# Kernel tuning notes

Measured on AMD Instinct MI355X. Metric: run time of the kernel, lower is better.

The kernel has to match this reference:

```python
import jax, jax.numpy as jnp
import numpy as np

B, L, D = 2048, 200, 256
N_USERS, N_ATTRS, N_RATINGS = 100000, 50000, 5


def setup_inputs() -> dict:
    key = jax.random.key(0)
    ks = jax.random.split(key, 16)
    s = 0.02
    return {
        "nodes": jax.random.randint(ks[0], (B,), 0, N_USERS),
        "history_ua": jax.random.randint(ks[1], (B, L), 0, N_ATTRS),
        "history_r": jax.random.randint(ks[2], (B, L), 0, N_RATINGS),
        "history_uat": jax.random.randint(ks[3], (B, L), 0, 512),
        "u2e_w": jax.random.normal(ks[4], (N_USERS, D), jnp.float32) * s,
        "attr_w": jax.random.normal(ks[5], (N_ATTRS, D), jnp.float32) * s,
        "r2e_w": jax.random.normal(ks[6], (N_RATINGS, D), jnp.float32) * s,
        "w_r1_w": jax.random.normal(ks[7], (D, 2 * D), jnp.float32) * s,
        "w_r1_b": jnp.zeros((D,), jnp.float32),
        "w_r2_w": jax.random.normal(ks[8], (D, D), jnp.float32) * s,
        "w_r2_b": jnp.zeros((D,), jnp.float32),
        "att1_w": jax.random.normal(ks[9], (D, 2 * D), jnp.float32) * s,
        "att1_b": jnp.zeros((D,), jnp.float32),
        "att2_w": jax.random.normal(ks[10], (D, D), jnp.float32) * s,
        "att2_b": jnp.zeros((D,), jnp.float32),
        "att3_w": jax.random.normal(ks[11], (1, D), jnp.float32) * s,
        "att3_b": jnp.zeros((1,), jnp.float32),
    }


def reference(nodes, history_ua, history_r, history_uat,
              u2e_w, attr_w, r2e_w,
              w_r1_w, w_r1_b, w_r2_w, w_r2_b,
              att1_w, att1_b, att2_w, att2_b, att3_w, att3_b):
    # gathers: e_ua [B,L,D], e_r [B,L,D], ua_rep [B,D]
    e_ua = attr_w[history_ua]
    e_r = r2e_w[history_r]
    ua_rep = u2e_w[nodes]
    # o_history = relu(w_r2(relu(w_r1(cat(e_ua, e_r)))))  [B,L,D]
    x = jnp.concatenate([e_ua, e_r], axis=-1)            # [B,L,2D]
    x = jax.nn.relu(jnp.einsum('bld,kd->blk', x, w_r1_w) + w_r1_b)
    o = jax.nn.relu(jnp.einsum('bld,kd->blk', x, w_r2_w) + w_r2_b)
    # attention: MLP on cat(o_history, ua_rep) -> softmax over history dim
    a = jnp.concatenate([o, jnp.broadcast_to(ua_rep[:, None, :], o.shape)], axis=-1)  # [B,L,2D]
    h = jax.nn.relu(jnp.einsum('bld,kd->blk', a, att1_w) + att1_b)
    h = jax.nn.relu(jnp.einsum('bld,kd->blk', h, att2_w) + att2_b)
    score = jnp.einsum('bld,kd->blk', h, att3_w) + att3_b  # [B,L,1]
    att = jax.nn.softmax(score, axis=1)
    # weighted reduce: o^T @ att per node -> [B,D]
    return jnp.sum(o * att, axis=1)
```

## Files before the change

kernel.cpp:

```cpp
#include <hip/hip_runtime.h>
#include <hip/hip_bf16.h>

typedef __bf16 bf16;
typedef __bf16 bf16x8 __attribute__((ext_vector_type(8)));
typedef float f32x4 __attribute__((ext_vector_type(4)));

#define L_SZ 200
#define D_SZ 256
#define NROWS (2048 * 200)
#define MB 128
#define MB2 64
#define AST 264
#define N_ATTR 50000
#define NPB ((N_ATTR + MB - 1) / MB)

#define WS_W2F 0u
#define WS_A1L 131072u
#define WS_A1H 262144u
#define WS_A2F 393216u
#define WS_W1A 524288u
#define WS_W1F 655360u
#define WS_R   917504u
#define WS_H1P 925696u
#define WS_SCR 3022848u
#define WS_O   4661248u
#define WS_P   214376448u
#define WS_NEED_OLD 214376448u
#define WS_NEED_NEW 239976448u

__device__ __forceinline__ void swz_one(const float* __restrict__ W, bf16* __restrict__ dst,
                                        int KT, int ldw, int koff, int g) {
    int lane = g & 63;
    int kt = (g >> 6) % KT;
    int nt = g / (64 * KT);
    int n = nt * 16 + (lane & 15);
    int k = kt * 32 + (lane >> 4) * 8;
    const float* src = W + (long)n * ldw + koff + k;
    f32x4 a = *(const f32x4*)src;
    f32x4 b = *(const f32x4*)(src + 4);
    bf16x8 v;
    v[0] = (bf16)a[0]; v[1] = (bf16)a[1]; v[2] = (bf16)a[2]; v[3] = (bf16)a[3];
    v[4] = (bf16)b[0]; v[5] = (bf16)b[1]; v[6] = (bf16)b[2]; v[7] = (bf16)b[3];
    *(bf16x8*)(dst + (long)g * 8) = v;
}

__global__ void swizzle_kernel(const float* __restrict__ W, bf16* __restrict__ dst,
                               int KT, int ldw, int koff, int total) {
    int g = blockIdx.x * blockDim.x + threadIdx.x;
    if (g >= total) return;
    swz_one(W, dst, KT, ldw, koff, g);
}

__global__ void swizzle_all(const float* __restrict__ w2, const float* __restrict__ a1w,
                            const float* __restrict__ a2w, const float* __restrict__ w1,
                            bf16* __restrict__ wf_w2, bf16* __restrict__ wf_a1l,
                            bf16* __restrict__ wf_a2f, bf16* __restrict__ wf_a1h,
                            bf16* __restrict__ wf_w1a,
                            const float* __restrict__ r2e, const float* __restrict__ b1w,
                            float* __restrict__ Rg) {
    __shared__ float e[5 * D_SZ];
    const int blk = blockIdx.x, t = threadIdx.x;
    if (blk == 160) {
        for (int i = t; i < 5 * D_SZ; i += 256) e[i] = r2e[i];
        __syncthreads();
        const float* wr = w1 + (long)t * 512 + 256;
        float bb = b1w[t];
        for (int r = 0; r < 5; ++r) {
            float a = bb;
            const float* er = e + r * D_SZ;
#pragma unroll
            for (int k = 0; k < D_SZ; k += 4) {
                f32x4 wv = *(const f32x4*)(wr + k);
                a += er[k] * wv[0] + er[k + 1] * wv[1] + er[k + 2] * wv[2] + er[k + 3] * wv[3];
            }
            Rg[r * D_SZ + t] = a;
        }
        return;
    }
    int job = blk >> 5, lb = blk & 31;
    int g = lb * 256 + t;
    const float* W; bf16* dst; int ldw, koff;
    switch (job) {
        case 0:  W = w2;  dst = wf_w2;  ldw = 256; koff = 0;   break;
        case 1:  W = a1w; dst = wf_a1l; ldw = 512; koff = 0;   break;
        case 2:  W = a2w; dst = wf_a2f; ldw = 256; koff = 0;   break;
        case 3:  W = a1w; dst = wf_a1h; ldw = 512; koff = 256; break;
        default: W = w1;  dst = wf_w1a; ldw = 512; koff = 0;   break;
    }
    swz_one(W, dst, 8, ldw, koff, g);
}

__device__ __forceinline__ void stage_rows(const int* __restrict__ idxl,
                                           const float* __restrict__ table,
                                           bf16* __restrict__ buf, int t) {
#pragma unroll
    for (int it = 0; it < 16; ++it) {
        int g = it * 256 + t;
        int r = g >> 5;
        int c = g & 31;
        long row = idxl[r];
        const float* f = table + row * D_SZ + c * 8;
        f32x4 a = *(const f32x4*)f;
        f32x4 b = *(const f32x4*)(f + 4);
        bf16x8 v;
        v[0] = (bf16)a[0]; v[1] = (bf16)a[1]; v[2] = (bf16)a[2]; v[3] = (bf16)a[3];
        v[4] = (bf16)b[0]; v[5] = (bf16)b[1]; v[6] = (bf16)b[2]; v[7] = (bf16)b[3];
        *(bf16x8*)(buf + r * AST + c * 8) = v;
    }
}

template <int MT, int KTOT>
__device__ __forceinline__ void gemm_t(const bf16* __restrict__ abase,
                                       const bf16* __restrict__ wfrag, int koff_t,
                                       int wave, int lane, int l16, int quad,
                                       f32x4 (&acc)[MT][4]) {
    const bf16* wbase = wfrag + ((long)(wave * 4) * KTOT + koff_t) * 512 + lane * 8;
    bf16x8 bc[4], bn[4];
#pragma unroll
    for (int nt = 0; nt < 4; ++nt)
        bc[nt] = *(const bf16x8*)(wbase + (long)nt * KTOT * 512);
#pragma unroll
    for (int kt = 0; kt < 8; ++kt) {
        if (kt < 7) {
#pragma unroll
            for (int nt = 0; nt < 4; ++nt)
                bn[nt] = *(const bf16x8*)(wbase + ((long)nt * KTOT + kt + 1) * 512);
        }
        bf16x8 a[MT];
#pragma unroll
        for (int mt = 0; mt < MT; ++mt)
            a[mt] = *(const bf16x8*)(abase + (mt * 16 + l16) * AST + kt * 32 + quad * 8);
#pragma unroll
        for (int nt = 0; nt < 4; ++nt)
#pragma unroll
            for (int mt = 0; mt < MT; ++mt)
                acc[mt][nt] = __builtin_amdgcn_mfma_f32_16x16x32_bf16(a[mt], bc[nt], acc[mt][nt], 0, 0, 0);
#pragma unroll
        for (int nt = 0; nt < 4; ++nt) bc[nt] = bn[nt];
    }
}

template <int MT>
__device__ __forceinline__ void zero_t(f32x4 (&acc)[MT][4]) {
    f32x4 z = {0.f, 0.f, 0.f, 0.f};
#pragma unroll
    for (int mt = 0; mt < MT; ++mt)
#pragma unroll
        for (int nt = 0; nt < 4; ++nt) acc[mt][nt] = z;
}

template <int MT>
__device__ __forceinline__ void store_act_t(bf16* __restrict__ buf, f32x4 (&acc)[MT][4],
                                            const float* bias, int wave, int l16, int quad) {
#pragma unroll
    for (int mt = 0; mt < MT; ++mt)
#pragma unroll
        for (int nt = 0; nt < 4; ++nt) {
            int col = (wave * 4 + nt) * 16 + l16;
#pragma unroll
            for (int r = 0; r < 4; ++r) {
                int row = mt * 16 + quad * 4 + r;
                float v = acc[mt][nt][r] + bias[nt];
                v = v > 0.f ? v : 0.f;
                buf[row * AST + col] = (bf16)v;
            }
        }
}

__device__ __forceinline__ void store_lin8(bf16* __restrict__ buf, f32x4 (&acc)[8][4],
                                           int wave, int l16, int quad) {
#pragma unroll
    for (int mt = 0; mt < 8; ++mt)
#pragma unroll
        for (int nt = 0; nt < 4; ++nt) {
            int col = (wave * 4 + nt) * 16 + l16;
#pragma unroll
            for (int r = 0; r < 4; ++r) {
                int row = mt * 16 + quad * 4 + r;
                buf[row * AST + col] = (bf16)acc[mt][nt][r];
            }
        }
}

__launch_bounds__(256, 2)
__global__ void kpre_k0(const float* __restrict__ attr, const bf16* __restrict__ wf_w1a,
                        bf16* __restrict__ Pt,
                        const int* __restrict__ nodes, const float* __restrict__ u2e,
                        const bf16* __restrict__ wf_a1h, const float* __restrict__ a1b,
                        float* __restrict__ h1p) {
    __shared__ __align__(16) bf16 abuf[MB * AST];
    __shared__ int idxl[MB];
    const int blk = blockIdx.x, t = threadIdx.x;
    const int wave = t >> 6, lane = t & 63, l16 = t & 15, quad = (t & 63) >> 4;
    const bool isP = blk < NPB;
    if (t < MB) {
        if (isP) { int r = blk * MB + t; idxl[t] = r < N_ATTR ? r : (N_ATTR - 1); }
        else idxl[t] = nodes[(blk - NPB) * MB + t];
    }
    __syncthreads();
    stage_rows(idxl, isP ? attr : u2e, abuf, t);
    __syncthreads();
    f32x4 acc[8][4];
    zero_t<8>(acc);
    gemm_t<8, 8>(abuf, isP ? wf_w1a : wf_a1h, 0, wave, lane, l16, quad, acc);
    if (isP) {
        __syncthreads();
        store_lin8(abuf, acc, wave, l16, quad);
        __syncthreads();
#pragma unroll
        for (int it = 0; it < 16; ++it) {
            int g = it * 256 + t;
            int r = g >> 5, c = g & 31;
            long row = (long)blk * MB + r;
            if (row < N_ATTR)
                *(bf16x8*)(Pt + row * D_SZ + c * 8) = *(const bf16x8*)(abuf + r * AST + c * 8);
        }
    } else {
        const int blk0 = blk - NPB;
#pragma unroll
        for (int nt = 0; nt < 4; ++nt) {
            int col = (wave * 4 + nt) * 16 + l16;
            float ab = a1b[col];
#pragma unroll
            for (int mt = 0; mt < 8; ++mt)
#pragma unroll
                for (int r = 0; r < 4; ++r) {
                    int row = mt * 16 + quad * 4 + r;
                    h1p[(long)(blk0 * MB + row) * D_SZ + col] = acc[mt][nt][r] + ab;
                }
        }
    }
}

__launch_bounds__(256, 2)
__global__ void k0_h1pre(const int* __restrict__ nodes, const float* __restrict__ u2e,
                         const bf16* __restrict__ wf_a1h, const float* __restrict__ a1b,
                         float* __restrict__ h1p) {
    __shared__ __align__(16) bf16 abuf[MB * AST];
    __shared__ int idxl[MB];
    const int blk = blockIdx.x, t = threadIdx.x;
    const int wave = t >> 6, lane = t & 63, l16 = t & 15, quad = (t & 63) >> 4;
    if (t < MB) idxl[t] = nodes[blk * MB + t];
    __syncthreads();
    stage_rows(idxl, u2e, abuf, t);
    __syncthreads();
    f32x4 acc[8][4];
    zero_t<8>(acc);
    gemm_t<8, 8>(abuf, wf_a1h, 0, wave, lane, l16, quad, acc);
#pragma unroll
    for (int nt = 0; nt < 4; ++nt) {
        int col = (wave * 4 + nt) * 16 + l16;
        float ab = a1b[col];
#pragma unroll
        for (int mt = 0; mt < 8; ++mt)
#pragma unroll
            for (int r = 0; r < 4; ++r) {
                int row = mt * 16 + quad * 4 + r;
                h1p[(long)(blk * MB + row) * D_SZ + col] = acc[mt][nt][r] + ab;
            }
    }
}

__launch_bounds__(256, 4)
__global__ void k1f_fused(const int* __restrict__ hua, const int* __restrict__ hr,
                          const bf16* __restrict__ Pt, const float* __restrict__ Rg,
                          const bf16* __restrict__ wf_w2, const bf16* __restrict__ wf_a1l,
                          const bf16* __restrict__ wf_a2f, const float* __restrict__ h1p,
                          const float* __restrict__ b2w, const float* __restrict__ a2b,
                          const float* __restrict__ a3w,
                          bf16* __restrict__ o_out, float* __restrict__ scores) {
    __shared__ __align__(16) bf16 abuf[MB2 * AST];
    __shared__ int idx_ua[MB2], idx_r[MB2];
    __shared__ float Rl[5 * D_SZ];
    __shared__ float spart[4][MB2];
    const int blk = blockIdx.x, t = threadIdx.x;
    const int wave = t >> 6, lane = t & 63, l16 = t & 15, quad = (t & 63) >> 4;
    const long r0 = (long)blk * MB2;
    const int b0 = (int)(r0 / L_SZ);
    const int b1i = min(b0 + 1, 2047);
    const long bsplit = (long)(b0 + 1) * L_SZ;
    if (t < MB2) { idx_ua[t] = hua[r0 + t]; idx_r[t] = hr[r0 + t]; }
    for (int i = t; i < 5 * D_SZ; i += 256) Rl[i] = Rg[i];
    __syncthreads();
#pragma unroll
    for (int it = 0; it < 4; ++it) {
        int g = it * 256 + t;
        int r = g >> 4, c = g & 15;
        long row = idx_ua[r];
        const bf16* pp = Pt + row * D_SZ + c * 16;
        bf16x8 v0 = *(const bf16x8*)pp;
        bf16x8 v1 = *(const bf16x8*)(pp + 8);
        const float* Rr = Rl + idx_r[r] * D_SZ + c * 16;
        f32x4 ra = *(const f32x4*)(Rr);
        f32x4 rb = *(const f32x4*)(Rr + 4);
        f32x4 rc = *(const f32x4*)(Rr + 8);
        f32x4 rd = *(const f32x4*)(Rr + 12);
        bf16x8 o0, o1;
#pragma unroll
        for (int j = 0; j < 4; ++j) {
            float a = (float)v0[j] + ra[j];
            float b = (float)v0[j + 4] + rb[j];
            float cc = (float)v1[j] + rc[j];
            float d = (float)v1[j + 4] + rd[j];
            o0[j]     = (bf16)(a > 0.f ? a : 0.f);
            o0[j + 4] = (bf16)(b > 0.f ? b : 0.f);
            o1[j]     = (bf16)(cc > 0.f ? cc : 0.f);
            o1[j + 4] = (bf16)(d > 0.f ? d : 0.f);
        }
        *(bf16x8*)(abuf + r * AST + c * 16) = o0;
        *(bf16x8*)(abuf + r * AST + c * 16 + 8) = o1;
    }
    __syncthreads();

    f32x4 acc[4][4];
    zero_t<4>(acc);
    gemm_t<4, 8>(abuf, wf_w2, 0, wave, lane, l16, quad, acc);
    __syncthreads();
    float bias2[4];
#pragma unroll
    for (int nt = 0; nt < 4; ++nt) bias2[nt] = b2w[(wave * 4 + nt) * 16 + l16];
    store_act_t<4>(abuf, acc, bias2, wave, l16, quad);
    __syncthreads();
#pragma unroll
    for (int it = 0; it < 8; ++it) {
        int g = it * 256 + t;
        int r = g >> 5, c = g & 31;
        *(bf16x8*)(o_out + (r0 + r) * D_SZ + c * 8) = *(const bf16x8*)(abuf + r * AST + c * 8);
    }
    zero_t<4>(acc);
    gemm_t<4, 8>(abuf, wf_a1l, 0, wave, lane, l16, quad, acc);
    __syncthreads();
    float h0v[4], h1v[4];
#pragma unroll
    for (int nt = 0; nt < 4; ++nt) {
        int col = (wave * 4 + nt) * 16 + l16;
        h0v[nt] = h1p[(long)b0 * D_SZ + col];
        h1v[nt] = h1p[(long)b1i * D_SZ + col];
    }
#pragma unroll
    for (int nt = 0; nt < 4; ++nt) {
        int col = (wave * 4 + nt) * 16 + l16;
#pragma unroll
        for (int mt = 0; mt < 4; ++mt)
#pragma unroll
            for (int r = 0; r < 4; ++r) {
                int row = mt * 16 + quad * 4 + r;
                float bias = ((r0 + row) >= bsplit) ? h1v[nt] : h0v[nt];
                float v = acc[mt][nt][r] + bias;
                v = v > 0.f ? v : 0.f;
                abuf[row * AST + col] = (bf16)v;
            }
    }
    __syncthreads();
    zero_t<4>(acc);
    gemm_t<4, 8>(abuf, wf_a2f, 0, wave, lane, l16, quad, acc);

    float bias4[4], a3[4];
#pragma unroll
    for (int nt = 0; nt < 4; ++nt) {
        int col = (wave * 4 + nt) * 16 + l16;
        bias4[nt] = a2b[col];
        a3[nt] = a3w[col];
    }
    float p[4][4];
#pragma unroll
    for (int mt = 0; mt < 4; ++mt)
#pragma unroll
        for (int r = 0; r < 4; ++r) {
            float s = 0.f;
#pragma unroll
            for (int nt = 0; nt < 4; ++nt) {
                float h = acc[mt][nt][r] + bias4[nt];
                h = h > 0.f ? h : 0.f;
                s += h * a3[nt];
            }
            p[mt][r] = s;
        }
#pragma unroll
    for (int off = 1; off < 16; off <<= 1)
#pragma unroll
        for (int mt = 0; mt < 4; ++mt)
#pragma unroll
            for (int r = 0; r < 4; ++r) p[mt][r] += __shfl_xor(p[mt][r], off, 16);
    if (l16 == 0) {
#pragma unroll
        for (int mt = 0; mt < 4; ++mt)
#pragma unroll
            for (int r = 0; r < 4; ++r)
                spart[wave][mt * 16 + quad * 4 + r] = p[mt][r];
    }
    __syncthreads();
    if (t < MB2)
        scores[r0 + t] = spart[0][t] + spart[1][t] + spart[2][t] + spart[3][t];
}

__launch_bounds__(256, 2)
__global__ void k1_gemm12(const int* __restrict__ hua, const int* __restrict__ hr,
                          const float* __restrict__ attr, const float* __restrict__ r2e,
                          const bf16* __restrict__ wf_w1, const bf16* __restrict__ wf_w2,
                          const float* __restrict__ b1w, const float* __restrict__ b2w,
                          bf16* __restrict__ o_out) {
    __shared__ __align__(16) bf16 abuf[MB * AST];
    __shared__ int idx_ua[MB], idx_r[MB];
    const int blk = blockIdx.x, t = threadIdx.x;
    const int wave = t >> 6, lane = t & 63, l16 = t & 15, quad = (t & 63) >> 4;
    const long r0 = (long)blk * MB;
    if (t < MB) { idx_ua[t] = hua[r0 + t]; idx_r[t] = hr[r0 + t]; }
    __syncthreads();

    float bias1[4], bias2[4];
#pragma unroll
    for (int nt = 0; nt < 4; ++nt) {
        int col = (wave * 4 + nt) * 16 + l16;
        bias1[nt] = b1w[col];
        bias2[nt] = b2w[col];
    }

    f32x4 acc[8][4];
    zero_t<8>(acc);
    stage_rows(idx_ua, attr, abuf, t);
    __syncthreads();
    gemm_t<8, 16>(abuf, wf_w1, 0, wave, lane, l16, quad, acc);
    __syncthreads();
    stage_rows(idx_r, r2e, abuf, t);
    __syncthreads();
    gemm_t<8, 16>(abuf, wf_w1, 8, wave, lane, l16, quad, acc);
    __syncthreads();
    store_act_t<8>(abuf, acc, bias1, wave, l16, quad);
    __syncthreads();
    zero_t<8>(acc);
    gemm_t<8, 8>(abuf, wf_w2, 0, wave, lane, l16, quad, acc);
    __syncthreads();
    store_act_t<8>(abuf, acc, bias2, wave, l16, quad);
    __syncthreads();
#pragma unroll
    for (int it = 0; it < 16; ++it) {
        int g = it * 256 + t;
        int r = g >> 5, c = g & 31;
        *(bf16x8*)(o_out + (r0 + r) * D_SZ + c * 8) = *(const bf16x8*)(abuf + r * AST + c * 8);
    }
}

__launch_bounds__(256, 2)
__global__ void k2_gemm34(const bf16* __restrict__ o_in,
                          const bf16* __restrict__ wf_a1l, const bf16* __restrict__ wf_a2f,
                          const float* __restrict__ h1p, const float* __restrict__ a2b,
                          const float* __restrict__ a3w, float* __restrict__ scores) {
    __shared__ __align__(16) bf16 abuf[MB * AST];
    __shared__ float hp[2][D_SZ];
    __shared__ float spart[4][MB];
    const int blk = blockIdx.x, t = threadIdx.x;
    const int wave = t >> 6, lane = t & 63, l16 = t & 15, quad = (t & 63) >> 4;
    const long r0 = (long)blk * MB;
    const int b0 = (int)(r0 / L_SZ);
    const int b1 = min(b0 + 1, 2047);
    const long bsplit = (long)(b0 + 1) * L_SZ;
    hp[0][t] = h1p[(long)b0 * D_SZ + t];
    hp[1][t] = h1p[(long)b1 * D_SZ + t];
#pragma unroll
    for (int it = 0; it < 16; ++it) {
        int g = it * 256 + t;
        int r = g >> 5, c = g & 31;
        *(bf16x8*)(abuf + r * AST + c * 8) = *(const bf16x8*)(o_in + (r0 + r) * D_SZ + c * 8);
    }
    __syncthreads();

    f32x4 acc[8][4];
    zero_t<8>(acc);
    gemm_t<8, 8>(abuf, wf_a1l, 0, wave, lane, l16, quad, acc);
    __syncthreads();
#pragma unroll
    for (int nt = 0; nt < 4; ++nt) {
        int col = (wave * 4 + nt) * 16 + l16;
#pragma unroll
        for (int mt = 0; mt < 8; ++mt)
#pragma unroll
            for (int r = 0; r < 4; ++r) {
                int row = mt * 16 + quad * 4 + r;
                float bias = ((r0 + row) >= bsplit) ? hp[1][col] : hp[0][col];
                float v = acc[mt][nt][r] + bias;
                v = v > 0.f ? v : 0.f;
                abuf[row * AST + col] = (bf16)v;
            }
    }
    __syncthreads();
    zero_t<8>(acc);
    gemm_t<8, 8>(abuf, wf_a2f, 0, wave, lane, l16, quad, acc);

    float bias4[4], a3[4];
#pragma unroll
    for (int nt = 0; nt < 4; ++nt) {
        int col = (wave * 4 + nt) * 16 + l16;
        bias4[nt] = a2b[col];
        a3[nt] = a3w[col];
    }
    float p[8][4];
#pragma unroll
    for (int mt = 0; mt < 8; ++mt)
#pragma unroll
        for (int r = 0; r < 4; ++r) {
            float s = 0.f;
#pragma unroll
            for (int nt = 0; nt < 4; ++nt) {
                float h = acc[mt][nt][r] + bias4[nt];
                h = h > 0.f ? h : 0.f;
                s += h * a3[nt];
            }
            p[mt][r] = s;
        }
#pragma unroll
    for (int off = 1; off < 16; off <<= 1)
#pragma unroll
        for (int mt = 0; mt < 8; ++mt)
#pragma unroll
            for (int r = 0; r < 4; ++r) p[mt][r] += __shfl_xor(p[mt][r], off, 16);
    if (l16 == 0) {
#pragma unroll
        for (int mt = 0; mt < 8; ++mt)
#pragma unroll
            for (int r = 0; r < 4; ++r)
                spart[wave][mt * 16 + quad * 4 + r] = p[mt][r];
    }
    __syncthreads();
    if (t < MB)
        scores[r0 + t] = spart[0][t] + spart[1][t] + spart[2][t] + spart[3][t];
}

__global__ void k5_reduce(const float* __restrict__ scores, const bf16* __restrict__ o_in,
                          float* __restrict__ out) {
    __shared__ float red[256];
    __shared__ float watt[256];
    __shared__ float racc[8][264];
    const int b = blockIdx.x, t = threadIdx.x;
    float s = (t < L_SZ) ? scores[(long)b * L_SZ + t] : -INFINITY;
    red[t] = s;
    __syncthreads();
    for (int off = 128; off > 0; off >>= 1) {
        if (t < off) red[t] = fmaxf(red[t], red[t + off]);
        __syncthreads();
    }
    float mx = red[0];
    __syncthreads();
    float w = (t < L_SZ) ? __expf(s - mx) : 0.f;
    watt[t] = w;
    red[t] = w;
    __syncthreads();
    for (int off = 128; off > 0; off >>= 1) {
        if (t < off) red[t] += red[t + off];
        __syncthreads();
    }
    float inv = 1.f / red[0];
    const int c8 = t & 31, rg = t >> 5;
    f32x4 a0 = {0.f, 0.f, 0.f, 0.f}, a1 = {0.f, 0.f, 0.f, 0.f};
    const bf16* ob = o_in + (long)b * L_SZ * D_SZ + c8 * 8;
#pragma unroll 5
    for (int l = rg; l < L_SZ; l += 8) {
        float wv = watt[l];
        bf16x8 v = *(const bf16x8*)(ob + (long)l * D_SZ);
        a0[0] += wv * (float)v[0]; a0[1] += wv * (float)v[1];
        a0[2] += wv * (float)v[2]; a0[3] += wv * (float)v[3];
        a1[0] += wv * (float)v[4]; a1[1] += wv * (float)v[5];
        a1[2] += wv * (float)v[6]; a1[3] += wv * (float)v[7];
    }
    *(f32x4*)(&racc[rg][c8 * 8]) = a0;
    *(f32x4*)(&racc[rg][c8 * 8 + 4]) = a1;
    __syncthreads();
    float r2 = 0.f;
#pragma unroll
    for (int g = 0; g < 8; ++g) r2 += racc[g][t];
    out[(long)b * D_SZ + t] = r2 * inv;
}

__device__ __forceinline__ void gather_half_f(const int* __restrict__ idxp,
                                              const float* __restrict__ table,
                                              bf16* __restrict__ buf, int l0, int t) {
#pragma unroll
    for (int it = 0; it < 6; ++it) {
        int g = it * 256 + t;
        int r = g >> 5, c = g & 31;
        int l = l0 + r;
        int li = l < L_SZ ? l : (L_SZ - 1);
        long row = idxp[li];
        const float* f = table + row * D_SZ + c * 8;
        f32x4 a = *(const f32x4*)f;
        f32x4 b2 = *(const f32x4*)(f + 4);
        bf16x8 v;
        v[0] = (bf16)a[0]; v[1] = (bf16)a[1]; v[2] = (bf16)a[2]; v[3] = (bf16)a[3];
        v[4] = (bf16)b2[0]; v[5] = (bf16)b2[1]; v[6] = (bf16)b2[2]; v[7] = (bf16)b2[3];
        *(bf16x8*)(buf + r * AST + c * 8) = v;
    }
}

__launch_bounds__(256, 3)
__global__ void ua_fused(const int* __restrict__ nodes, const int* __restrict__ hua,
                         const int* __restrict__ hr, const float* __restrict__ u2e,
                         const float* __restrict__ attr, const float* __restrict__ r2e,
                         const bf16* __restrict__ wf1, const bf16* __restrict__ wf2,
                         const bf16* __restrict__ wfa1, const bf16* __restrict__ wfa2,
                         const float* __restrict__ b1w, const float* __restrict__ b2w,
                         const float* __restrict__ att1w, const float* __restrict__ a1b,
                         const float* __restrict__ a2b, const float* __restrict__ att3w,
                         const float* __restrict__ a3bp, float* __restrict__ out) {
    __shared__ __align__(16) bf16 abuf[48 * AST];
    __shared__ __align__(16) bf16 obuf[48 * AST];
    __shared__ float h1pre[D_SZ];
    __shared__ float scratch[288];
    const int b = blockIdx.x, t = threadIdx.x;
    const int wave = t >> 6, lane = t & 63, l16 = t & 15, quad = (t & 63) >> 4;
    {
        int node = nodes[b];
        scratch[t] = u2e[(long)node * D_SZ + t];
        __syncthreads();
        float a = a1b[t];
        const float* wr = att1w + (long)t * 512 + 256;
#pragma unroll
        for (int k = 0; k < 256; k += 4) {
            f32x4 wv = *(const f32x4*)(wr + k);
            a += scratch[k] * wv[0] + scratch[k + 1] * wv[1] +
                 scratch[k + 2] * wv[2] + scratch[k + 3] * wv[3];
        }
        h1pre[t] = a;
        __syncthreads();
    }
    float bias1[4], bias2[4], bias3[4], bias4[4], a3[4];
#pragma unroll
    for (int nt = 0; nt < 4; ++nt) {
        int col = (wave * 4 + nt) * 16 + l16;
        bias1[nt] = b1w[col]; bias2[nt] = b2w[col]; bias3[nt] = h1pre[col];
        bias4[nt] = a2b[col]; a3[nt] = att3w[col];
    }
    const float a3bias = a3bp[0];
    const int* huab = hua + (long)b * L_SZ;
    const int* hrb = hr + (long)b * L_SZ;
    float accv = 0.f, srun = 0.f, mrun = -INFINITY;
    float* score_part = scratch;
    float* score_row = scratch + 192;
    float* wrow = scratch + 240;
    auto st3 = [&](bf16* buf, f32x4 (&acc)[3][4], const float* bias) {
#pragma unroll
        for (int mt = 0; mt < 3; ++mt)
#pragma unroll
            for (int nt = 0; nt < 4; ++nt) {
                int col = (wave * 4 + nt) * 16 + l16;
#pragma unroll
                for (int r = 0; r < 4; ++r) {
                    float v = acc[mt][nt][r] + bias[nt];
                    v = v > 0.f ? v : 0.f;
                    buf[(mt * 16 + quad * 4 + r) * AST + col] = (bf16)v;
                }
            }
    };
    for (int tile = 0; tile < 5; ++tile) {
        const int l0 = tile * 48;
        f32x4 acc[3][4];
        zero_t<3>(acc);
        gather_half_f(huab, attr, abuf, l0, t);
        __syncthreads();
        gemm_t<3, 16>(abuf, wf1, 0, wave, lane, l16, quad, acc);
        __syncthreads();
        gather_half_f(hrb, r2e, abuf, l0, t);
        __syncthreads();
        gemm_t<3, 16>(abuf, wf1, 8, wave, lane, l16, quad, acc);
        __syncthreads();
        st3(abuf, acc, bias1);
        __syncthreads();
        zero_t<3>(acc);
        gemm_t<3, 8>(abuf, wf2, 0, wave, lane, l16, quad, acc);
        st3(obuf, acc, bias2);
        __syncthreads();
        zero_t<3>(acc);
        gemm_t<3, 8>(obuf, wfa1, 0, wave, lane, l16, quad, acc);
        st3(abuf, acc, bias3);
        __syncthreads();
        zero_t<3>(acc);
        gemm_t<3, 8>(abuf, wfa2, 0, wave, lane, l16, quad, acc);
        float p[3][4];
#pragma unroll
        for (int mt = 0; mt < 3; ++mt)
#pragma unroll
            for (int r = 0; r < 4; ++r) {
                float s = 0.f;
#pragma unroll
                for (int nt = 0; nt < 4; ++nt) {
                    float h = acc[mt][nt][r] + bias4[nt];
                    h = h > 0.f ? h : 0.f;
                    s += h * a3[nt];
                }
                p[mt][r] = s;
            }
#pragma unroll
        for (int off = 1; off < 16; off <<= 1)
#pragma unroll
            for (int mt = 0; mt < 3; ++mt)
#pragma unroll
                for (int r = 0; r < 4; ++r) p[mt][r] += __shfl_xor(p[mt][r], off, 16);
        if (l16 == 0) {
#pragma unroll
            for (int mt = 0; mt < 3; ++mt)
#pragma unroll
                for (int r = 0; r < 4; ++r)
                    score_part[wave * 48 + mt * 16 + quad * 4 + r] = p[mt][r];
        }
        __syncthreads();
        if (t < 48) {
            float s = score_part[t] + score_part[48 + t] + score_part[96 + t] +
                      score_part[144 + t] + a3bias;
            score_row[t] = (l0 + t < L_SZ) ? s : -INFINITY;
        }
        __syncthreads();
        float tm = -INFINITY;
        for (int r = 0; r < 48; ++r) tm = fmaxf(tm, score_row[r]);
        float nm = fmaxf(mrun, tm);
        float factor = __expf(mrun - nm);
        if (t < 48) wrow[t] = __expf(score_row[t] - nm);
        __syncthreads();
        float wsum = 0.f, av = 0.f;
#pragma unroll 8
        for (int r = 0; r < 48; ++r) {
            float w = wrow[r];
            wsum += w;
            av += w * (float)obuf[r * AST + t];
        }
        accv = accv * factor + av;
        srun = srun * factor + wsum;
        mrun = nm;
        __syncthreads();
    }
    out[(long)b * D_SZ + t] = accv / srun;
}

extern "C" void kernel_launch(void* const* d_in, const int* in_sizes, int n_in,
                              void* d_out, int out_size, void* d_ws, size_t ws_size,
                              hipStream_t stream) {
    const int* nodes = (const int*)d_in[0];
    const int* hua = (const int*)d_in[1];
    const int* hr = (const int*)d_in[2];
    const float* u2e = (const float*)d_in[4];
    const float* attr = (const float*)d_in[5];
    const float* r2e = (const float*)d_in[6];
    const float* w1 = (const float*)d_in[7];
    const float* b1 = (const float*)d_in[8];
    const float* w2 = (const float*)d_in[9];
    const float* b2 = (const float*)d_in[10];
    const float* a1w = (const float*)d_in[11];
    const float* a1b = (const float*)d_in[12];
    const float* a2w = (const float*)d_in[13];
    const float* a2b = (const float*)d_in[14];
    const float* a3w = (const float*)d_in[15];
    const float* a3b = (const float*)d_in[16];
    char* ws = (char*)d_ws;
    bf16* wf_w2 = (bf16*)(ws + WS_W2F);
    bf16* wf_a1l = (bf16*)(ws + WS_A1L);
    bf16* wf_a1h = (bf16*)(ws + WS_A1H);
    bf16* wf_a2f = (bf16*)(ws + WS_A2F);
    bf16* wf_w1a = (bf16*)(ws + WS_W1A);
    bf16* wf_w1 = (bf16*)(ws + WS_W1F);

    if (ws_size >= (size_t)WS_NEED_NEW) {
        float* Rg = (float*)(ws + WS_R);
        float* h1p = (float*)(ws + WS_H1P);
        float* scores = (float*)(ws + WS_SCR);
        bf16* obuf = (bf16*)(ws + WS_O);
        bf16* Pt = (bf16*)(ws + WS_P);
        swizzle_all<<<161, 256, 0, stream>>>(w2, a1w, a2w, w1,
                                             wf_w2, wf_a1l, wf_a2f, wf_a1h, wf_w1a,
                                             r2e, b1, Rg);
        kpre_k0<<<NPB + 2048 / MB, 256, 0, stream>>>(attr, wf_w1a, Pt,
                                                     nodes, u2e, wf_a1h, a1b, h1p);
        k1f_fused<<<NROWS / MB2, 256, 0, stream>>>(hua, hr, Pt, Rg, wf_w2, wf_a1l,
                                                   wf_a2f, h1p, b2, a2b, a3w,
                                                   obuf, scores);
        k5_reduce<<<2048, 256, 0, stream>>>(scores, obuf, (float*)d_out);
    } else if (ws_size >= (size_t)WS_NEED_OLD) {
        float* h1p = (float*)(ws + WS_H1P);
        float* scores = (float*)(ws + WS_SCR);
        bf16* obuf = (bf16*)(ws + WS_O);
        swizzle_kernel<<<32, 256, 0, stream>>>(w2, wf_w2, 8, 256, 0, 8192);
        swizzle_kernel<<<32, 256, 0, stream>>>(a1w, wf_a1l, 8, 512, 0, 8192);
        swizzle_kernel<<<32, 256, 0, stream>>>(a2w, wf_a2f, 8, 256, 0, 8192);
        swizzle_kernel<<<64, 256, 0, stream>>>(w1, wf_w1, 16, 512, 0, 16384);
        swizzle_kernel<<<32, 256, 0, stream>>>(a1w, wf_a1h, 8, 512, 256, 8192);
        k0_h1pre<<<2048 / MB, 256, 0, stream>>>(nodes, u2e, wf_a1h, a1b, h1p);
        k1_gemm12<<<NROWS / MB, 256, 0, stream>>>(hua, hr, attr, r2e, wf_w1, wf_w2,
                                                  b1, b2, obuf);
        k2_gemm34<<<NROWS / MB, 256, 0, stream>>>(obuf, wf_a1l, wf_a2f, h1p, a2b,
                                                  a3w, scores);
        k5_reduce<<<2048, 256, 0, stream>>>(scores, obuf, (float*)d_out);
    } else {
        swizzle_kernel<<<32, 256, 0, stream>>>(w2, wf_w2, 8, 256, 0, 8192);
        swizzle_kernel<<<32, 256, 0, stream>>>(a1w, wf_a1l, 8, 512, 0, 8192);
        swizzle_kernel<<<32, 256, 0, stream>>>(a2w, wf_a2f, 8, 256, 0, 8192);
        swizzle_kernel<<<64, 256, 0, stream>>>(w1, wf_w1, 16, 512, 0, 16384);
        ua_fused<<<2048, 256, 0, stream>>>(nodes, hua, hr, u2e, attr, r2e,
                                           wf_w1, wf_w2, wf_a1l, wf_a2f,
                                           b1, b2, a1w, a1b, a2b, a3w, a3b,
                                           (float*)d_out);
    }
}
```

Measured before the change: 526.5 us.

## Fuse softmax-weighted reduction into fused kernel via per-block partial stats

The fused MLP kernel no longer writes the bf16 o_history buffer and per-row scores to global memory. Each 64-row block now keeps o in packed registers, computes a local max and exp-sum for each of the two batch segments it spans, and writes weighted partial sums plus stats. A small combine kernel merges these flash-style into the output. The precompute kernel also moves to 64-row tiles with direct fp32→bf16 staging and higher occupancy, and the fused kernel reads R from global memory instead of LDS. The cost is extra registers for the packed o copy and the added shuffle reductions.

New measurement: 576.6 us. 1.1x slower.

```diff
diff --git a/kernel.cpp b/kernel.cpp
--- a/kernel.cpp
+++ b/kernel.cpp
@@ -13,6 +13,8 @@
 #define AST 264
 #define N_ATTR 50000
 #define NPB ((N_ATTR + MB - 1) / MB)
+#define NPB64 ((N_ATTR + MB2 - 1) / MB2)
+#define NK0 (2048 / MB2)
 
 #define WS_W2F 0u
 #define WS_A1L 131072u
@@ -24,9 +26,21 @@
 #define WS_H1P 925696u
 #define WS_SCR 3022848u
 #define WS_O   4661248u
+#define WS_PART 4661248u
+#define WS_STAT 17768448u
 #define WS_P   214376448u
 #define WS_NEED_OLD 214376448u
 #define WS_NEED_NEW 239976448u
+
+__device__ __forceinline__ unsigned pack2(float a, float b) {
+    unsigned short ua = __builtin_bit_cast(unsigned short, (bf16)a);
+    unsigned short ub = __builtin_bit_cast(unsigned short, (bf16)b);
+    return (unsigned)ua | ((unsigned)ub << 16);
+}
+__device__ __forceinline__ float unpk(unsigned v, int hi) {
+    unsigned short u = hi ? (unsigned short)(v >> 16) : (unsigned short)(v & 0xffff);
+    return (float)__builtin_bit_cast(bf16, u);
+}
 
 __device__ __forceinline__ void swz_one(const float* __restrict__ W, bf16* __restrict__ dst,
                                         int KT, int ldw, int koff, int g) {
@@ -167,10 +181,32 @@
         }
 }
 
-__device__ __forceinline__ void store_lin8(bf16* __restrict__ buf, f32x4 (&acc)[8][4],
-                                           int wave, int l16, int quad) {
-#pragma unroll
-    for (int mt = 0; mt < 8; ++mt)
+__device__ __forceinline__ void store_act_pack4(bf16* __restrict__ buf, f32x4 (&acc)[4][4],
+                                                const float* bias, unsigned (&obak)[4][4][2],
+                                                int wave, int l16, int quad) {
+#pragma unroll
+    for (int mt = 0; mt < 4; ++mt)
+#pragma unroll
+        for (int nt = 0; nt < 4; ++nt) {
+            int col = (wave * 4 + nt) * 16 + l16;
+            float v[4];
+#pragma unroll
+            for (int r = 0; r < 4; ++r) {
+                float x = acc[mt][nt][r] + bias[nt];
+                v[r] = x > 0.f ? x : 0.f;
+                int row = mt * 16 + quad * 4 + r;
+                buf[row * AST + col] = (bf16)v[r];
+            }
+            obak[mt][nt][0] = pack2(v[0], v[1]);
+            obak[mt][nt][1] = pack2(v[2], v[3]);
+        }
+}
+
+template <int MT>
+__device__ __forceinline__ void store_lin_t(bf16* __restrict__ buf, f32x4 (&acc)[MT][4],
+                                            int wave, int l16, int quad) {
+#pragma unroll
+    for (int mt = 0; mt < MT; ++mt)
 #pragma unroll
         for (int nt = 0; nt < 4; ++nt) {
             int col = (wave * 4 + nt) * 16 + l16;
@@ -182,54 +218,274 @@
         }
 }
 
-__launch_bounds__(256, 2)
+__launch_bounds__(256, 4)
 __global__ void kpre_k0(const float* __restrict__ attr, const bf16* __restrict__ wf_w1a,
                         bf16* __restrict__ Pt,
                         const int* __restrict__ nodes, const float* __restrict__ u2e,
                         const bf16* __restrict__ wf_a1h, const float* __restrict__ a1b,
                         float* __restrict__ h1p) {
-    __shared__ __align__(16) bf16 abuf[MB * AST];
-    __shared__ int idxl[MB];
+    __shared__ __align__(16) bf16 abuf[MB2 * AST];
     const int blk = blockIdx.x, t = threadIdx.x;
     const int wave = t >> 6, lane = t & 63, l16 = t & 15, quad = (t & 63) >> 4;
-    const bool isP = blk < NPB;
-    if (t < MB) {
-        if (isP) { int r = blk * MB + t; idxl[t] = r < N_ATTR ? r : (N_ATTR - 1); }
-        else idxl[t] = nodes[(blk - NPB) * MB + t];
-    }
-    __syncthreads();
-    stage_rows(idxl, isP ? attr : u2e, abuf, t);
-    __syncthreads();
-    f32x4 acc[8][4];
-    zero_t<8>(acc);
-    gemm_t<8, 8>(abuf, isP ? wf_w1a : wf_a1h, 0, wave, lane, l16, quad, acc);
+    const bool isP = blk < NPB64;
+    const int blk0 = blk - NPB64;
+    const float* table = isP ? attr : u2e;
+#pragma unroll
+    for (int it = 0; it < 8; ++it) {
+        int g = it * 256 + t;
+        int r = g >> 5, c = g & 31;
+        long row;
+        if (isP) { row = (long)blk * MB2 + r; if (row >= N_ATTR) row = N_ATTR - 1; }
+        else row = nodes[blk0 * MB2 + r];
+        const float* f = table + row * D_SZ + c * 8;
+        f32x4 a = *(const f32x4*)f;
+        f32x4 b = *(const f32x4*)(f + 4);
+        bf16x8 v;
+        v[0] = (bf16)a[0]; v[1] = (bf16)a[1]; v[2] = (bf16)a[2]; v[3] = (bf16)a[3];
+        v[4] = (bf16)b[0]; v[5] = (bf16)b[1]; v[6] = (bf16)b[2]; v[7] = (bf16)b[3];
+        *(bf16x8*)(abuf + r * AST + c * 8) = v;
+    }
+    __syncthreads();
+    f32x4 acc[4][4];
+    zero_t<4>(acc);
+    gemm_t<4, 8>(abuf, isP ? wf_w1a : wf_a1h, 0, wave, lane, l16, quad, acc);
     if (isP) {
         __syncthreads();
-        store_lin8(abuf, acc, wave, l16, quad);
-        __syncthreads();
-#pragma unroll
-        for (int it = 0; it < 16; ++it) {
+        store_lin_t<4>(abuf, acc, wave, l16, quad);
+        __syncthreads();
+#pragma unroll
+        for (int it = 0; it < 8; ++it) {
             int g = it * 256 + t;
             int r = g >> 5, c = g & 31;
-            long row = (long)blk * MB + r;
+            long row = (long)blk * MB2 + r;
             if (row < N_ATTR)
                 *(bf16x8*)(Pt + row * D_SZ + c * 8) = *(const bf16x8*)(abuf + r * AST + c * 8);
         }
     } else {
-        const int blk0 = blk - NPB;
 #pragma unroll
         for (int nt = 0; nt < 4; ++nt) {
             int col = (wave * 4 + nt) * 16 + l16;
             float ab = a1b[col];
 #pragma unroll
-            for (int mt = 0; mt < 8; ++mt)
+            for (int mt = 0; mt < 4; ++mt)
 #pragma unroll
                 for (int r = 0; r < 4; ++r) {
                     int row = mt * 16 + quad * 4 + r;
-                    h1p[(long)(blk0 * MB + row) * D_SZ + col] = acc[mt][nt][r] + ab;
+                    h1p[(long)(blk0 * MB2 + row) * D_SZ + col] = acc[mt][nt][r] + ab;
                 }
         }
     }
+}
+
+__launch_bounds__(256, 4)
+__global__ void k1f_fused(const int* __restrict__ hua, const int* __restrict__ hr,
+                          const bf16* __restrict__ Pt, const float* __restrict__ Rg,
+                          const bf16* __restrict__ wf_w2, const bf16* __restrict__ wf_a1l,
+                          const bf16* __restrict__ wf_a2f, const float* __restrict__ h1p,
+                          const float* __restrict__ b2w, const float* __restrict__ a2b,
+                          const float* __restrict__ a3w,
+                          float* __restrict__ parts, float* __restrict__ stats) {
+    __shared__ __align__(16) bf16 abuf[MB2 * AST];
+    __shared__ int idx_ua[MB2], idx_r[MB2];
+    __shared__ float spart[4][MB2];
+    __shared__ float wLA[MB2], wLB[MB2];
+    const int blk = blockIdx.x, t = threadIdx.x;
+    const int wave = t >> 6, lane = t & 63, l16 = t & 15, quad = (t & 63) >> 4;
+    const long r0 = (long)blk * MB2;
+    const int b0 = (int)(r0 / L_SZ);
+    const int b1i = min(b0 + 1, 2047);
+    const long bsplit = (long)(b0 + 1) * L_SZ;
+    if (t < MB2) { idx_ua[t] = hua[r0 + t]; idx_r[t] = hr[r0 + t]; }
+    __syncthreads();
+#pragma unroll
+    for (int it = 0; it < 4; ++it) {
+        int g = it * 256 + t;
+        int r = g >> 4, c = g & 15;
+        long row = idx_ua[r];
+        const bf16* pp = Pt + row * D_SZ + c * 16;
+        bf16x8 v0 = *(const bf16x8*)pp;
+        bf16x8 v1 = *(const bf16x8*)(pp + 8);
+        const float* Rr = Rg + idx_r[r] * D_SZ + c * 16;
+        f32x4 ra = *(const f32x4*)(Rr);
+        f32x4 rb = *(const f32x4*)(Rr + 4);
+        f32x4 rc = *(const f32x4*)(Rr + 8);
+        f32x4 rd = *(const f32x4*)(Rr + 12);
+        bf16x8 o0, o1;
+#pragma unroll
+        for (int j = 0; j < 4; ++j) {
+            float a = (float)v0[j] + ra[j];
+            float b = (float)v0[j + 4] + rb[j];
+            float cc = (float)v1[j] + rc[j];
+            float d = (float)v1[j + 4] + rd[j];
+            o0[j]     = (bf16)(a > 0.f ? a : 0.f);
+            o0[j + 4] = (bf16)(b > 0.f ? b : 0.f);
+            o1[j]     = (bf16)(cc > 0.f ? cc : 0.f);
+            o1[j + 4] = (bf16)(d > 0.f ? d : 0.f);
+        }
+        *(bf16x8*)(abuf + r * AST + c * 16) = o0;
+        *(bf16x8*)(abuf + r * AST + c * 16 + 8) = o1;
+    }
+    __syncthreads();
+
+    f32x4 acc[4][4];
+    unsigned obak[4][4][2];
+    zero_t<4>(acc);
+    gemm_t<4, 8>(abuf, wf_w2, 0, wave, lane, l16, quad, acc);
+    __syncthreads();
+    float bias2[4];
+#pragma unroll
+    for (int nt = 0; nt < 4; ++nt) bias2[nt] = b2w[(wave * 4 + nt) * 16 + l16];
+    store_act_pack4(abuf, acc, bias2, obak, wave, l16, quad);
+    __syncthreads();
+    zero_t<4>(acc);
+    gemm_t<4, 8>(abuf, wf_a1l, 0, wave, lane, l16, quad, acc);
+    __syncthreads();
+    float h0v[4], h1v[4];
+#pragma unroll
+    for (int nt = 0; nt < 4; ++nt) {
+        int col = (wave * 4 + nt) * 16 + l16;
+        h0v[nt] = h1p[(long)b0 * D_SZ + col];
+        h1v[nt] = h1p[(long)b1i * D_SZ + col];
+    }
+#pragma unroll
+    for (int nt = 0; nt < 4; ++nt) {
+        int col = (wave * 4 + nt) * 16 + l16;
+#pragma unroll
+        for (int mt = 0; mt < 4; ++mt)
+#pragma unroll
+            for (int r = 0; r < 4; ++r) {
+                int row = mt * 16 + quad * 4 + r;
+                float bias = ((r0 + row) >= bsplit) ? h1v[nt] : h0v[nt];
+                float v = acc[mt][nt][r] + bias;
+                v = v > 0.f ? v : 0.f;
+                abuf[row * AST + col] = (bf16)v;
+            }
+    }
+    __syncthreads();
+    zero_t<4>(acc);
+    gemm_t<4, 8>(abuf, wf_a2f, 0, wave, lane, l16, quad, acc);
+
+    float bias4[4], a3[4];
+#pragma unroll
+    for (int nt = 0; nt < 4; ++nt) {
+        int col = (wave * 4 + nt) * 16 + l16;
+        bias4[nt] = a2b[col];
+        a3[nt] = a3w[col];
+    }
+    float p[4][4];
+#pragma unroll
+    for (int mt = 0; mt < 4; ++mt)
+#pragma unroll
+        for (int r = 0; r < 4; ++r) {
+            float s = 0.f;
+#pragma unroll
+            for (int nt = 0; nt < 4; ++nt) {
+                float h = acc[mt][nt][r] + bias4[nt];
+                h = h > 0.f ? h : 0.f;
+                s += h * a3[nt];
+            }
+            p[mt][r] = s;
+        }
+#pragma unroll
+    for (int off = 1; off < 16; off <<= 1)
+#pragma unroll
+        for (int mt = 0; mt < 4; ++mt)
+#pragma unroll
+            for (int r = 0; r < 4; ++r) p[mt][r] += __shfl_xor(p[mt][r], off, 16);
+    if (l16 == 0) {
+#pragma unroll
+        for (int mt = 0; mt < 4; ++mt)
+#pragma unroll
+            for (int r = 0; r < 4; ++r)
+                spart[wave][mt * 16 + quad * 4 + r] = p[mt][r];
+    }
+    __syncthreads();
+    if (t < MB2) {
+        float sc = spart[0][t] + spart[1][t] + spart[2][t] + spart[3][t];
+        bool isB = (r0 + t) >= bsplit;
+        float sA = isB ? -INFINITY : sc;
+        float sB = isB ? sc : -INFINITY;
+        float mA = sA, mB = sB;
+#pragma unroll
+        for (int off = 1; off < 64; off <<= 1) {
+            mA = fmaxf(mA, __shfl_xor(mA, off, 64));
+            mB = fmaxf(mB, __shfl_xor(mB, off, 64));
+        }
+        float wa = isB ? 0.f : __expf(sc - mA);
+        float wb = isB ? __expf(sc - mB) : 0.f;
+        float ssA = wa, ssB = wb;
+#pragma unroll
+        for (int off = 1; off < 64; off <<= 1) {
+            ssA += __shfl_xor(ssA, off, 64);
+            ssB += __shfl_xor(ssB, off, 64);
+        }
+        wLA[t] = wa;
+        wLB[t] = wb;
+        if (t == 0) {
+            stats[(long)blk * 4 + 0] = mA;
+            stats[(long)blk * 4 + 1] = ssA;
+            stats[(long)blk * 4 + 2] = mB;
+            stats[(long)blk * 4 + 3] = ssB;
+        }
+    }
+    __syncthreads();
+    float psA[4] = {0.f, 0.f, 0.f, 0.f}, psB[4] = {0.f, 0.f, 0.f, 0.f};
+#pragma unroll
+    for (int mt = 0; mt < 4; ++mt)
+#pragma unroll
+        for (int rr = 0; rr < 4; ++rr) {
+            int row = mt * 16 + quad * 4 + rr;
+            float wa = wLA[row], wb = wLB[row];
+#pragma unroll
+            for (int nt = 0; nt < 4; ++nt) {
+                float ov = unpk(obak[mt][nt][rr >> 1], rr & 1);
+                psA[nt] += wa * ov;
+                psB[nt] += wb * ov;
+            }
+        }
+#pragma unroll
+    for (int nt = 0; nt < 4; ++nt) {
+        psA[nt] += __shfl_xor(psA[nt], 16, 64);
+        psA[nt] += __shfl_xor(psA[nt], 32, 64);
+        psB[nt] += __shfl_xor(psB[nt], 16, 64);
+        psB[nt] += __shfl_xor(psB[nt], 32, 64);
+    }
+    if (quad == 0) {
+#pragma unroll
+        for (int nt = 0; nt < 4; ++nt)
+            parts[((long)blk * 2 + 0) * D_SZ + wave * 64 + nt * 16 + l16] = psA[nt];
+    } else if (quad == 1) {
+#pragma unroll
+        for (int nt = 0; nt < 4; ++nt)
+            parts[((long)blk * 2 + 1) * D_SZ + wave * 64 + nt * 16 + l16] = psB[nt];
+    }
+}
+
+__global__ void kc_combine(const float* __restrict__ parts, const float* __restrict__ stats,
+                           float* __restrict__ out) {
+    const int b = blockIdx.x, t = threadIdx.x;
+    const int k0 = (b * L_SZ) / MB2;
+    float m[4], s[4];
+    int seg[4];
+    float M = -INFINITY;
+#pragma unroll
+    for (int i = 0; i < 4; ++i) {
+        int k = k0 + i;
+        int bA = (k * MB2) / L_SZ;
+        int sg = (bA == b) ? 0 : 1;
+        seg[i] = sg;
+        m[i] = stats[(long)k * 4 + sg * 2];
+        s[i] = stats[(long)k * 4 + sg * 2 + 1];
+        M = fmaxf(M, m[i]);
+    }
+    float denom = 0.f, accv = 0.f;
+#pragma unroll
+    for (int i = 0; i < 4; ++i) {
+        float f = __expf(m[i] - M);
+        denom += f * s[i];
+        accv += f * parts[((long)(k0 + i) * 2 + seg[i]) * D_SZ + t];
+    }
+    out[(long)b * D_SZ + t] = accv / denom;
 }
 
 __launch_bounds__(256, 2)
@@ -259,139 +515,6 @@
                 h1p[(long)(blk * MB + row) * D_SZ + col] = acc[mt][nt][r] + ab;
             }
     }
-}
-
-__launch_bounds__(256, 4)
-__global__ void k1f_fused(const int* __restrict__ hua, const int* __restrict__ hr,
-                          const bf16* __restrict__ Pt, const float* __restrict__ Rg,
-                          const bf16* __restrict__ wf_w2, const bf16* __restrict__ wf_a1l,
-                          const bf16* __restrict__ wf_a2f, const float* __restrict__ h1p,
-                          const float* __restrict__ b2w, const float* __restrict__ a2b,
-                          const float* __restrict__ a3w,
-                          bf16* __restrict__ o_out, float* __restrict__ scores) {
-    __shared__ __align__(16) bf16 abuf[MB2 * AST];
-    __shared__ int idx_ua[MB2], idx_r[MB2];
-    __shared__ float Rl[5 * D_SZ];
-    __shared__ float spart[4][MB2];
-    const int blk = blockIdx.x, t = threadIdx.x;
-    const int wave = t >> 6, lane = t & 63, l16 = t & 15, quad = (t & 63) >> 4;
-    const long r0 = (long)blk * MB2;
-    const int b0 = (int)(r0 / L_SZ);
-    const int b1i = min(b0 + 1, 2047);
-    const long bsplit = (long)(b0 + 1) * L_SZ;
-    if (t < MB2) { idx_ua[t] = hua[r0 + t]; idx_r[t] = hr[r0 + t]; }
-    for (int i = t; i < 5 * D_SZ; i += 256) Rl[i] = Rg[i];
-    __syncthreads();
-#pragma unroll
-    for (int it = 0; it < 4; ++it) {
-        int g = it * 256 + t;
-        int r = g >> 4, c = g & 15;
-        long row = idx_ua[r];
-        const bf16* pp = Pt + row * D_SZ + c * 16;
-        bf16x8 v0 = *(const bf16x8*)pp;
-        bf16x8 v1 = *(const bf16x8*)(pp + 8);
-        const float* Rr = Rl + idx_r[r] * D_SZ + c * 16;
-        f32x4 ra = *(const f32x4*)(Rr);
-        f32x4 rb = *(const f32x4*)(Rr + 4);
-        f32x4 rc = *(const f32x4*)(Rr + 8);
-        f32x4 rd = *(const f32x4*)(Rr + 12);
-        bf16x8 o0, o1;
-#pragma unroll
-        for (int j = 0; j < 4; ++j) {
-            float a = (float)v0[j] + ra[j];
-            float b = (float)v0[j + 4] + rb[j];
-            float cc = (float)v1[j] + rc[j];
-            float d = (float)v1[j + 4] + rd[j];
-            o0[j]     = (bf16)(a > 0.f ? a : 0.f);
-            o0[j + 4] = (bf16)(b > 0.f ? b : 0.f);
-            o1[j]     = (bf16)(cc > 0.f ? cc : 0.f);
-            o1[j + 4] = (bf16)(d > 0.f ? d : 0.f);
-        }
-        *(bf16x8*)(abuf + r * AST + c * 16) = o0;
-        *(bf16x8*)(abuf + r * AST + c * 16 + 8) = o1;
-    }
-    __syncthreads();
-
-    f32x4 acc[4][4];
-    zero_t<4>(acc);
-    gemm_t<4, 8>(abuf, wf_w2, 0, wave, lane, l16, quad, acc);
-    __syncthreads();
-    float bias2[4];
-#pragma unroll
-    for (int nt = 0; nt < 4; ++nt) bias2[nt] = b2w[(wave * 4 + nt) * 16 + l16];
-    store_act_t<4>(abuf, acc, bias2, wave, l16, quad);
-    __syncthreads();
-#pragma unroll
-    for (int it = 0; it < 8; ++it) {
-        int g = it * 256 + t;
-        int r = g >> 5, c = g & 31;
-        *(bf16x8*)(o_out + (r0 + r) * D_SZ + c * 8) = *(const bf16x8*)(abuf + r * AST + c * 8);
-    }
-    zero_t<4>(acc);
-    gemm_t<4, 8>(abuf, wf_a1l, 0, wave, lane, l16, quad, acc);
-    __syncthreads();
-    float h0v[4], h1v[4];
-#pragma unroll
-    for (int nt = 0; nt < 4; ++nt) {
-        int col = (wave * 4 + nt) * 16 + l16;
-        h0v[nt] = h1p[(long)b0 * D_SZ + col];
-        h1v[nt] = h1p[(long)b1i * D_SZ + col];
-    }
-#pragma unroll
-    for (int nt = 0; nt < 4; ++nt) {
-        int col = (wave * 4 + nt) * 16 + l16;
-#pragma unroll
-        for (int mt = 0; mt < 4; ++mt)
-#pragma unroll
-            for (int r = 0; r < 4; ++r) {
-                int row = mt * 16 + quad * 4 + r;
-                float bias = ((r0 + row) >= bsplit) ? h1v[nt] : h0v[nt];
-                float v = acc[mt][nt][r] + bias;
-                v = v > 0.f ? v : 0.f;
-                abuf[row * AST + col] = (bf16)v;
-            }
-    }
-    __syncthreads();
-    zero_t<4>(acc);
-    gemm_t<4, 8>(abuf, wf_a2f, 0, wave, lane, l16, quad, acc);
-
-    float bias4[4], a3[4];
-#pragma unroll
-    for (int nt = 0; nt < 4; ++nt) {
-        int col = (wave * 4 + nt) * 16 + l16;
-        bias4[nt] = a2b[col];
-        a3[nt] = a3w[col];
-    }
-    float p[4][4];
-#pragma unroll
-    for (int mt = 0; mt < 4; ++mt)
-#pragma unroll
-        for (int r = 0; r < 4; ++r) {
-            float s = 0.f;
-#pragma unroll
-            for (int nt = 0; nt < 4; ++nt) {
-                float h = acc[mt][nt][r] + bias4[nt];
-                h = h > 0.f ? h : 0.f;
-                s += h * a3[nt];
-            }
-            p[mt][r] = s;
-        }
-#pragma unroll
-    for (int off = 1; off < 16; off <<= 1)
-#pragma unroll
-        for (int mt = 0; mt < 4; ++mt)
-#pragma unroll
-            for (int r = 0; r < 4; ++r) p[mt][r] += __shfl_xor(p[mt][r], off, 16);
-    if (l16 == 0) {
-#pragma unroll
-        for (int mt = 0; mt < 4; ++mt)
-#pragma unroll
-            for (int r = 0; r < 4; ++r)
-                spart[wave][mt * 16 + quad * 4 + r] = p[mt][r];
-    }
-    __syncthreads();
-    if (t < MB2)
-        scores[r0 + t] = spart[0][t] + spart[1][t] + spart[2][t] + spart[3][t];
 }
 
 __launch_bounds__(256, 2)
@@ -759,18 +882,18 @@
     if (ws_size >= (size_t)WS_NEED_NEW) {
         float* Rg = (float*)(ws + WS_R);
         float* h1p = (float*)(ws + WS_H1P);
-        float* scores = (float*)(ws + WS_SCR);
-        bf16* obuf = (bf16*)(ws + WS_O);
+        float* parts = (float*)(ws + WS_PART);
+        float* stats = (float*)(ws + WS_STAT);
         bf16* Pt = (bf16*)(ws + WS_P);
         swizzle_all<<<161, 256, 0, stream>>>(w2, a1w, a2w, w1,
                                              wf_w2, wf_a1l, wf_a2f, wf_a1h, wf_w1a,
                                              r2e, b1, Rg);
-        kpre_k0<<<NPB + 2048 / MB, 256, 0, stream>>>(attr, wf_w1a, Pt,
-                                                     nodes, u2e, wf_a1h, a1b, h1p);
+        kpre_k0<<<NPB64 + NK0, 256, 0, stream>>>(attr, wf_w1a, Pt,
+                                                 nodes, u2e, wf_a1h, a1b, h1p);
         k1f_fused<<<NROWS / MB2, 256, 0, stream>>>(hua, hr, Pt, Rg, wf_w2, wf_a1l,
                                                    wf_a2f, h1p, b2, a2b, a3w,
-                                                   obuf, scores);
-        k5_reduce<<<2048, 256, 0, stream>>>(scores, obuf, (float*)d_out);
+                                                   parts, stats);
+        kc_combine<<<2048, 256, 0, stream>>>(parts, stats, (float*)d_out);
     } else if (ws_size >= (size_t)WS_NEED_OLD) {
         float* h1p = (float*)(ws + WS_H1P);
         float* scores = (float*)(ws + WS_SCR);
```
